# Performance work log

Hardware: AMD Instinct MI355X
Metric: run time of the kernel (lower is better)

Reference implementation:

```python
import jax, jax.numpy as jnp
import numpy as np

IN_F = 4096
OUT_F = 4096
B, S = 4, 2048
BITS = 4
N_LEVELS = 1 << BITS  # 16


def setup_inputs() -> dict:
    key = jax.random.key(0)
    kx, kr, ks, kb = jax.random.split(key, 4)
    x = jax.random.normal(kx, (B, S, IN_F), dtype=jnp.float32)
    # random orthogonal rotation (TurboQuantMSE rotation matrix, seeded)
    g = jax.random.normal(kr, (IN_F, IN_F), dtype=jnp.float32)
    rotation, _ = jnp.linalg.qr(g)
    # 4-bit scalar codebook: Lloyd-Max-style Gaussian levels, scaled for
    # unit-norm rows whose rotated entries ~ N(0, 1/in_features)
    p = (jnp.arange(N_LEVELS, dtype=jnp.float32) + 0.5) / N_LEVELS
    levels = jnp.sqrt(2.0) * jax.scipy.special.erfinv(2.0 * p - 1.0)
    codebook = (levels / jnp.sqrt(jnp.float32(IN_F))).astype(jnp.float32)
    weight_indices = jax.random.randint(jax.random.fold_in(key, 1), (OUT_F, IN_F), 0, N_LEVELS, dtype=jnp.int32)
    weight_scale = jax.random.uniform(ks, (OUT_F,), dtype=jnp.float32, minval=0.5, maxval=2.0)
    bias = jax.random.normal(kb, (OUT_F,), dtype=jnp.float32)
    return {"x": x, "weight_indices": weight_indices, "weight_scale": weight_scale,
            "bias": bias, "rotation": rotation, "codebook": codebook}


def reference(x, weight_indices, weight_scale, bias, rotation, codebook):
    # dequantize: codebook lookup -> inverse rotation -> per-row rescale
    w_rot = codebook[weight_indices]                      # (out, in)
    w_hat = jnp.einsum('oi,ji->oj', w_rot, rotation)      # apply R^T: (out, in)
    w = w_hat * weight_scale[:, None]                     # (out, in)
    # F.linear: x @ W^T + b
    return jnp.einsum('bsi,oi->bso', x, w) + bias
```

## Files before the change

### kernel.cpp

```cpp
#include <hip/hip_runtime.h>

typedef short short8 __attribute__((ext_vector_type(8)));
typedef float f32x4 __attribute__((ext_vector_type(4)));

#define GLOBAL_AS __attribute__((address_space(1)))
#define LDS_AS    __attribute__((address_space(3)))

__device__ __forceinline__ unsigned short f2bf(float f) {
    unsigned u = __builtin_bit_cast(unsigned, f);
    u += 0x7fffu + ((u >> 16) & 1u);
    return (unsigned short)(u >> 16);
}

__global__ __launch_bounds__(256) void k_idx2bf(const int* __restrict__ idx,
                                                const float* __restrict__ cb,
                                                ushort* __restrict__ out, int n4) {
    int i = blockIdx.x * 256 + threadIdx.x;
    if (i >= n4) return;
    int4 v = reinterpret_cast<const int4*>(idx)[i];
    ushort4 o;
    o.x = f2bf(cb[v.x]); o.y = f2bf(cb[v.y]);
    o.z = f2bf(cb[v.z]); o.w = f2bf(cb[v.w]);
    reinterpret_cast<ushort4*>(out)[i] = o;
}

__global__ __launch_bounds__(256) void k_f2bf(const float* __restrict__ in,
                                              ushort* __restrict__ out, int n4) {
    int i = blockIdx.x * 256 + threadIdx.x;
    if (i >= n4) return;
    float4 v = reinterpret_cast<const float4*>(in)[i];
    ushort4 o;
    o.x = f2bf(v.x); o.y = f2bf(v.y); o.z = f2bf(v.z); o.w = f2bf(v.w);
    reinterpret_cast<ushort4*>(out)[i] = o;
}


#define CH_AE(j) ((((j) & 8) << 1) | ((j) & 7))
#define CH_AL(j) (CH_AE(j) + 8)
#define CH_BE(j) ((((j) & 12) << 1) | ((j) & 3))
#define CH_BL(j) (CH_BE(j) + 4)

#define STAGE2(GB, LW, KB, CF) do {                                             \
    const int c0_ = CF(2 * w);                                                  \
    const int c1_ = CF(2 * w + 1);                                              \
    __builtin_amdgcn_global_load_lds(                                           \
        (const GLOBAL_AS void*)((GB) + (size_t)c0_ * 32768 + (KB)),             \
        (LDS_AS void*)((LW) + c0_ * 512), 16, 0, 0);                            \
    __builtin_amdgcn_global_load_lds(                                           \
        (const GLOBAL_AS void*)((GB) + (size_t)c1_ * 32768 + (KB)),             \
        (LDS_AS void*)((LW) + c1_ * 512), 16, 0, 0);                            \
} while (0)

#define READ_A(DST, BUF, MH) do {                                               \
    _Pragma("unroll")                                                           \
    for (int mi = 0; mi < 4; ++mi)                                              \
        DST[0][mi] = *reinterpret_cast<const short8*>(                          \
            sAc + ak0 + ((BUF) * 32768 + (MH) * 8192 + mi * 2048));             \
    _Pragma("unroll")                                                           \
    for (int mi = 0; mi < 4; ++mi)                                              \
        DST[1][mi] = *reinterpret_cast<const short8*>(                          \
            sAc + ak1 + ((BUF) * 32768 + (MH) * 8192 + mi * 2048));             \
} while (0)

#define READ_B(DST, BUF, NH) do {                                               \
    _Pragma("unroll")                                                           \
    for (int ni = 0; ni < 2; ++ni)                                              \
        DST[0][ni] = *reinterpret_cast<const short8*>(                          \
            sBc + bk0 + ((BUF) * 32768 + (NH) * 4096 + ni * 2048));             \
    _Pragma("unroll")                                                           \
    for (int ni = 0; ni < 2; ++ni)                                              \
        DST[1][ni] = *reinterpret_cast<const short8*>(                          \
            sBc + bk1 + ((BUF) * 32768 + (NH) * 4096 + ni * 2048));             \
} while (0)

#define MFMA16(MH, NH, AF, BF)                                                  \
    _Pragma("unroll")                                                           \
    for (int k2 = 0; k2 < 2; ++k2)                                              \
        _Pragma("unroll")                                                       \
        for (int mi = 0; mi < 4; ++mi)                                          \
            _Pragma("unroll")                                                   \
            for (int ni = 0; ni < 2; ++ni)                                      \
                acc[(MH) * 4 + mi][(NH) * 2 + ni] =                             \
                    __builtin_amdgcn_mfma_f32_16x16x32_bf16(                    \
                        AF[k2][mi], BF[k2][ni], acc[(MH) * 4 + mi][(NH) * 2 + ni], 0, 0, 0)

#define PH_MID do {                                                             \
    asm volatile("" ::: "memory");                                              \
    __builtin_amdgcn_s_barrier();                                               \
    asm volatile("s_waitcnt lgkmcnt(0)" ::: "memory");                          \
    __builtin_amdgcn_sched_barrier(0);                                          \
    __builtin_amdgcn_s_setprio(1);                                              \
} while (0)

#define PH_END do {                                                             \
    __builtin_amdgcn_s_setprio(0);                                              \
    asm volatile("" ::: "memory");                                              \
    __builtin_amdgcn_s_barrier();                                               \
    asm volatile("" ::: "memory");                                              \
} while (0)

#define PH1S(BUF, ...) do {                                                     \
    READ_A(aF, BUF, 0); READ_B(b0f, BUF, 0);                                    \
    __VA_ARGS__;                                                                \
    asm volatile("s_waitcnt lgkmcnt(8)" ::: "memory");                          \
    PH_MID; MFMA16(0, 0, aF, b0f); PH_END;                                      \
} while (0)

#define PH2S(BUF, ...) do {                                                     \
    READ_B(b1f, BUF, 1);                                                        \
    __VA_ARGS__;                                                                \
    PH_MID; MFMA16(0, 1, aF, b1f); PH_END;                                      \
} while (0)

#define PH3S(BUF, ...) do {                                                     \
    READ_A(aF, BUF, 1);                                                         \
    __VA_ARGS__;                                                                \
    PH_MID; MFMA16(1, 0, aF, b0f); PH_END;                                      \
} while (0)

#define PH4S(FN, ...) do {                                                      \
    __VA_ARGS__;                                                                \
    PH_MID; MFMA16(1, 1, aF, b1f);                                              \
    __builtin_amdgcn_s_setprio(0);                                              \
    asm volatile("s_waitcnt vmcnt(" #FN ")" ::: "memory");                      \
    __builtin_amdgcn_s_barrier();                                               \
    asm volatile("" ::: "memory");                                              \
} while (0)

#define PH4SNF(...) do {                                                        \
    __VA_ARGS__;                                                                \
    PH_MID; MFMA16(1, 1, aF, b1f); PH_END;                                      \
} while (0)

template <int EPI>
__global__ __launch_bounds__(512, 2) void gemm256(const ushort* __restrict__ A,
                                                  const ushort* __restrict__ B,
                                                  void* __restrict__ C,
                                                  const float* __restrict__ extra) {
    constexpr int K = 4096, N = 4096;
    __shared__ ushort sA[2][256 * 64];
    __shared__ ushort sB[2][256 * 64];

    const int tid  = threadIdx.x;
    const int w    = tid >> 6;
    const int lane = tid & 63;
    const int wm = w >> 2, wn = w & 3;

    const int nwg = gridDim.x;
    const int sw  = ((int)blockIdx.x & 7) * (nwg >> 3) + ((int)blockIdx.x >> 3);
    const int m0 = (sw >> 4) * 256;
    const int n0 = (sw & 15) * 256;

    const int srow8 = lane >> 3;
    const int scol  = (((lane & 7) ^ (lane >> 3)) * 8);
    const ushort* gAl = A + (size_t)m0 * K + srow8 * 4096 + scol;
    const ushort* gBl = B + (size_t)n0 * K + srow8 * 4096 + scol;

    const int fr   = lane & 15;
    const int fkb  = ((lane >> 4) & 3) * 16;
    const int swb  = (fr & 7) << 4;
    const int arow = wm * 128 + fr;
    const int brow = wn * 64 + fr;
    const char* sAc = (const char*)&sA[0][0];
    const char* sBc = (const char*)&sB[0][0];
    const int ak0 = (arow * 128 + 0  + fkb) ^ swb;
    const int ak1 = (arow * 128 + 64 + fkb) ^ swb;
    const int bk0 = (brow * 128 + 0  + fkb) ^ swb;
    const int bk1 = (brow * 128 + 64 + fkb) ^ swb;

    f32x4 acc[8][4];
#pragma unroll
    for (int i = 0; i < 8; ++i)
#pragma unroll
        for (int j = 0; j < 4; ++j) acc[i][j] = (f32x4){0.f, 0.f, 0.f, 0.f};

    short8 aF[2][4], b0f[2][2], b1f[2][2];

    STAGE2(gAl, sA[0], 0, CH_AE); STAGE2(gBl, sB[0], 0, CH_BE);
    STAGE2(gBl, sB[0], 0, CH_BL); STAGE2(gAl, sA[0], 0, CH_AL);
    STAGE2(gAl, sA[1], 64, CH_AE); STAGE2(gBl, sB[1], 64, CH_BE);
    STAGE2(gBl, sB[1], 64, CH_BL);
    asm volatile("s_waitcnt vmcnt(6)" ::: "memory");
    __builtin_amdgcn_s_barrier();
    asm volatile("" ::: "memory");

    for (int pr = 0; pr < 31; ++pr) {
        const int t = 2 * pr;
        const int kb1 = (t + 1) * 64, kb2 = (t + 2) * 64, kb3 = (t + 3) * 64;
        PH1S(0, STAGE2(gAl, sA[1], kb1, CH_AL));
        PH2S(0, STAGE2(gAl, sA[0], kb2, CH_AE));
        PH3S(0, STAGE2(gBl, sB[0], kb2, CH_BE));
        PH4S(6, STAGE2(gBl, sB[0], kb2, CH_BL));
        PH1S(1, STAGE2(gAl, sA[0], kb2, CH_AL));
        PH2S(1, STAGE2(gAl, sA[1], kb3, CH_AE));
        PH3S(1, STAGE2(gBl, sB[1], kb3, CH_BE));
        PH4S(6, STAGE2(gBl, sB[1], kb3, CH_BL));
    }
    {
        PH1S(0, STAGE2(gAl, sA[1], 63 * 64, CH_AL));
        PH2S(0, ((void)0));
        PH3S(0, ((void)0));
        PH4S(0, ((void)0));
        PH1S(1, ((void)0));
        PH2S(1, ((void)0));
        PH3S(1, ((void)0));
        PH4SNF(((void)0));
    }

    const int rb = m0 + wm * 128 + ((lane >> 4) * 4);
    const int cb = n0 + wn * 64 + (lane & 15);
    if (EPI == 0) {
        ushort* Cw = (ushort*)C;
#pragma unroll
        for (int mi = 0; mi < 8; ++mi) {
#pragma unroll
            for (int r = 0; r < 4; ++r) {
                const int row = rb + mi * 16 + r;
                const float s = extra[row];
#pragma unroll
                for (int ni = 0; ni < 4; ++ni)
                    Cw[(size_t)row * N + cb + ni * 16] = f2bf(acc[mi][ni][r] * s);
            }
        }
    } else {
        float* Cf = (float*)C;
#pragma unroll
        for (int ni = 0; ni < 4; ++ni) {
            const float b = extra[cb + ni * 16];
#pragma unroll
            for (int mi = 0; mi < 8; ++mi) {
#pragma unroll
                for (int r = 0; r < 4; ++r) {
                    const int row = rb + mi * 16 + r;
                    Cf[(size_t)row * N + cb + ni * 16] = acc[mi][ni][r] + b;
                }
            }
        }
    }
}

extern "C" void kernel_launch(void* const* d_in, const int* in_sizes, int n_in,
                              void* d_out, int out_size, void* d_ws, size_t ws_size,
                              hipStream_t stream) {
    const float* x     = (const float*)d_in[0];
    const int*   widx  = (const int*)  d_in[1];
    const float* wscal = (const float*)d_in[2];
    const float* bias  = (const float*)d_in[3];
    const float* rot   = (const float*)d_in[4];
    const float* cb    = (const float*)d_in[5];
    float* out = (float*)d_out;

    constexpr size_t IN_F = 4096, OUT_F = 4096, MTOK = 8192;
    char* ws = (char*)d_ws;
    ushort* wq   = (ushort*)(ws);
    ushort* rbuf = (ushort*)(ws + 33554432);
    ushort* xb   = (ushort*)(ws + 67108864);
    ushort* wb   = (ushort*)(ws + 134217728);
    (void)ws_size; (void)in_sizes; (void)n_in; (void)out_size;

    {
        int n4 = (int)(OUT_F * IN_F / 4);
        k_idx2bf<<<n4 / 256, 256, 0, stream>>>(widx, cb, wq, n4);
        k_f2bf<<<n4 / 256, 256, 0, stream>>>(rot, rbuf, n4);
        int n4x = (int)(MTOK * IN_F / 4);
        k_f2bf<<<n4x / 256, 256, 0, stream>>>(x, xb, n4x);
    }

    gemm256<0><<<dim3(256), 512, 0, stream>>>(wq, rbuf, (void*)wb, wscal);

    gemm256<1><<<dim3(512), 512, 0, stream>>>(xb, wb, (void*)out, bias);
}
```

Baseline: 453.8 us.

## Restructure GEMM main loop to one barrier per phase with simpler prefetch

```diff
diff --git a/kernel.cpp b/kernel.cpp
--- a/kernel.cpp
+++ b/kernel.cpp
@@ -55,25 +55,25 @@
     _Pragma("unroll")                                                           \
     for (int mi = 0; mi < 4; ++mi)                                              \
         DST[0][mi] = *reinterpret_cast<const short8*>(                          \
-            sAc + ak0 + ((BUF) * 32768 + (MH) * 8192 + mi * 2048));             \
+            sAc + ak0 + ((BUF) + (MH) * 8192 + mi * 2048));                     \
     _Pragma("unroll")                                                           \
     for (int mi = 0; mi < 4; ++mi)                                              \
         DST[1][mi] = *reinterpret_cast<const short8*>(                          \
-            sAc + ak1 + ((BUF) * 32768 + (MH) * 8192 + mi * 2048));             \
+            sAc + ak1 + ((BUF) + (MH) * 8192 + mi * 2048));                     \
 } while (0)
 
 #define READ_B(DST, BUF, NH) do {                                               \
     _Pragma("unroll")                                                           \
     for (int ni = 0; ni < 2; ++ni)                                              \
         DST[0][ni] = *reinterpret_cast<const short8*>(                          \
-            sBc + bk0 + ((BUF) * 32768 + (NH) * 4096 + ni * 2048));             \
+            sBc + bk0 + ((BUF) + (NH) * 4096 + ni * 2048));                     \
     _Pragma("unroll")                                                           \
     for (int ni = 0; ni < 2; ++ni)                                              \
         DST[1][ni] = *reinterpret_cast<const short8*>(                          \
-            sBc + bk1 + ((BUF) * 32768 + (NH) * 4096 + ni * 2048));             \
-} while (0)
-
-#define MFMA16(MH, NH, AF, BF)                                                  \
+            sBc + bk1 + ((BUF) + (NH) * 4096 + ni * 2048));                     \
+} while (0)
+
+#define MFMA16Q(MH, NH, AF, BF)                                                 \
     _Pragma("unroll")                                                           \
     for (int k2 = 0; k2 < 2; ++k2)                                              \
         _Pragma("unroll")                                                       \
@@ -84,52 +84,52 @@
                     __builtin_amdgcn_mfma_f32_16x16x32_bf16(                    \
                         AF[k2][mi], BF[k2][ni], acc[(MH) * 4 + mi][(NH) * 2 + ni], 0, 0, 0)
 
-#define PH_MID do {                                                             \
-    asm volatile("" ::: "memory");                                              \
-    __builtin_amdgcn_s_barrier();                                               \
-    asm volatile("s_waitcnt lgkmcnt(0)" ::: "memory");                          \
-    __builtin_amdgcn_sched_barrier(0);                                          \
-    __builtin_amdgcn_s_setprio(1);                                              \
-} while (0)
-
-#define PH_END do {                                                             \
-    __builtin_amdgcn_s_setprio(0);                                              \
-    asm volatile("" ::: "memory");                                              \
-    __builtin_amdgcn_s_barrier();                                               \
-    asm volatile("" ::: "memory");                                              \
-} while (0)
-
-#define PH1S(BUF, ...) do {                                                     \
+#define VMF(N) asm volatile("s_waitcnt vmcnt(" #N ")" ::: "memory")
+#define BARB   __builtin_amdgcn_s_barrier()
+
+#define PH1F(BUF, FN, ...) do {                                                 \
+    BARB;                                                                       \
+    __VA_ARGS__;                                                                \
+    __builtin_amdgcn_s_setprio(1);                                              \
     READ_A(aF, BUF, 0); READ_B(b0f, BUF, 0);                                    \
-    __VA_ARGS__;                                                                \
-    asm volatile("s_waitcnt lgkmcnt(8)" ::: "memory");                          \
-    PH_MID; MFMA16(0, 0, aF, b0f); PH_END;                                      \
-} while (0)
-
-#define PH2S(BUF, ...) do {                                                     \
+    MFMA16Q(0, 0, aF, b0f);                                                     \
+    __builtin_amdgcn_s_setprio(0);                                              \
+    VMF(FN);                                                                    \
+} while (0)
+
+#define PH2F(BUF, ...) do {                                                     \
+    BARB;                                                                       \
+    __VA_ARGS__;                                                                \
+    __builtin_amdgcn_s_setprio(1);                                              \
     READ_B(b1f, BUF, 1);                                                        \
-    __VA_ARGS__;                                                                \
-    PH_MID; MFMA16(0, 1, aF, b1f); PH_END;                                      \
-} while (0)
-
-#define PH3S(BUF, ...) do {                                                     \
+    MFMA16Q(0, 1, aF, b1f);                                                     \
+    __builtin_amdgcn_s_setprio(0);                                              \
+} while (0)
+
+#define PH3F(BUF, ...) do {                                                     \
+    BARB;                                                                       \
+    __VA_ARGS__;                                                                \
+    __builtin_amdgcn_s_setprio(1);                                              \
     READ_A(aF, BUF, 1);                                                         \
-    __VA_ARGS__;                                                                \
-    PH_MID; MFMA16(1, 0, aF, b0f); PH_END;                                      \
-} while (0)
-
-#define PH4S(FN, ...) do {                                                      \
-    __VA_ARGS__;                                                                \
-    PH_MID; MFMA16(1, 1, aF, b1f);                                              \
-    __builtin_amdgcn_s_setprio(0);                                              \
-    asm volatile("s_waitcnt vmcnt(" #FN ")" ::: "memory");                      \
-    __builtin_amdgcn_s_barrier();                                               \
-    asm volatile("" ::: "memory");                                              \
-} while (0)
-
-#define PH4SNF(...) do {                                                        \
-    __VA_ARGS__;                                                                \
-    PH_MID; MFMA16(1, 1, aF, b1f); PH_END;                                      \
+    MFMA16Q(1, 0, aF, b0f);                                                     \
+    __builtin_amdgcn_s_setprio(0);                                              \
+} while (0)
+
+#define PH4F(FN, ...) do {                                                      \
+    BARB;                                                                       \
+    __VA_ARGS__;                                                                \
+    __builtin_amdgcn_s_setprio(1);                                              \
+    MFMA16Q(1, 1, aF, b1f);                                                     \
+    __builtin_amdgcn_s_setprio(0);                                              \
+    VMF(FN);                                                                    \
+} while (0)
+
+#define PH4NO(...) do {                                                         \
+    BARB;                                                                       \
+    __VA_ARGS__;                                                                \
+    __builtin_amdgcn_s_setprio(1);                                              \
+    MFMA16Q(1, 1, aF, b1f);                                                     \
+    __builtin_amdgcn_s_setprio(0);                                              \
 } while (0)
 
 template <int EPI>
@@ -177,34 +177,30 @@
     short8 aF[2][4], b0f[2][2], b1f[2][2];
 
     STAGE2(gAl, sA[0], 0, CH_AE); STAGE2(gBl, sB[0], 0, CH_BE);
-    STAGE2(gBl, sB[0], 0, CH_BL); STAGE2(gAl, sA[0], 0, CH_AL);
-    STAGE2(gAl, sA[1], 64, CH_AE); STAGE2(gBl, sB[1], 64, CH_BE);
-    STAGE2(gBl, sB[1], 64, CH_BL);
-    asm volatile("s_waitcnt vmcnt(6)" ::: "memory");
-    __builtin_amdgcn_s_barrier();
-    asm volatile("" ::: "memory");
+    STAGE2(gAl, sA[0], 0, CH_AL); STAGE2(gBl, sB[0], 0, CH_BL);
+    VMF(2);
 
     for (int pr = 0; pr < 31; ++pr) {
         const int t = 2 * pr;
-        const int kb1 = (t + 1) * 64, kb2 = (t + 2) * 64, kb3 = (t + 3) * 64;
-        PH1S(0, STAGE2(gAl, sA[1], kb1, CH_AL));
-        PH2S(0, STAGE2(gAl, sA[0], kb2, CH_AE));
-        PH3S(0, STAGE2(gBl, sB[0], kb2, CH_BE));
-        PH4S(6, STAGE2(gBl, sB[0], kb2, CH_BL));
-        PH1S(1, STAGE2(gAl, sA[0], kb2, CH_AL));
-        PH2S(1, STAGE2(gAl, sA[1], kb3, CH_AE));
-        PH3S(1, STAGE2(gBl, sB[1], kb3, CH_BE));
-        PH4S(6, STAGE2(gBl, sB[1], kb3, CH_BL));
+        const int kb1 = (t + 1) * 64, kb2 = (t + 2) * 64;
+        PH1F(0, 2, STAGE2(gAl, sA[1], kb1, CH_AE));
+        PH2F(0,    STAGE2(gBl, sB[1], kb1, CH_BE));
+        PH3F(0,    STAGE2(gAl, sA[1], kb1, CH_AL));
+        PH4F(2,    STAGE2(gBl, sB[1], kb1, CH_BL));
+        PH1F(32768, 2, STAGE2(gAl, sA[0], kb2, CH_AE));
+        PH2F(32768,    STAGE2(gBl, sB[0], kb2, CH_BE));
+        PH3F(32768,    STAGE2(gAl, sA[0], kb2, CH_AL));
+        PH4F(2,        STAGE2(gBl, sB[0], kb2, CH_BL));
     }
     {
-        PH1S(0, STAGE2(gAl, sA[1], 63 * 64, CH_AL));
-        PH2S(0, ((void)0));
-        PH3S(0, ((void)0));
-        PH4S(0, ((void)0));
-        PH1S(1, ((void)0));
-        PH2S(1, ((void)0));
-        PH3S(1, ((void)0));
-        PH4SNF(((void)0));
+        PH1F(0, 2, STAGE2(gAl, sA[1], 4032, CH_AE));
+        PH2F(0,    STAGE2(gBl, sB[1], 4032, CH_BE));
+        PH3F(0,    STAGE2(gAl, sA[1], 4032, CH_AL));
+        PH4F(2,    STAGE2(gBl, sB[1], 4032, CH_BL));
+        PH1F(32768, 0, ((void)0));
+        PH2F(32768,    ((void)0));
+        PH3F(32768,    ((void)0));
+        PH4NO(((void)0));
     }
 
     const int rb = m0 + wm * 128 + ((lane >> 4) * 4);
```

Result: slower. 540.4 us (+19.1%).
